# Kernel tuning notes

Hardware: AMD Instinct MI355X
Metric: run time of the kernel (lower is better)

Reference implementation:

```python
import jax, jax.numpy as jnp
import numpy as np

B, T, C, H = 4, 1024, 1024, 16
D = C // H


def setup_inputs() -> dict:
    key = jax.random.key(0)
    ks = jax.random.split(key, 6)
    s = 1.0 / np.sqrt(C)
    return {
        "x": jax.random.normal(ks[0], (B, T, C), jnp.float32),
        "W_qkv": jax.random.normal(ks[1], (C, 3 * C), jnp.float32) * s,
        "b_qkv": jnp.zeros((3 * C,), jnp.float32),
        "W_out": jax.random.normal(ks[2], (C, C), jnp.float32) * s,
        "b_out": jnp.zeros((C,), jnp.float32),
        "w_sur": jax.random.normal(ks[3], (C,), jnp.float32) * s,
        "b_sur": jnp.zeros((), jnp.float32),
        "threshold": jnp.float32(0.5),
    }


def _expmap0_split(u):
    # geoopt Lorentz (k=1) expmap0: first coordinate is the time axis.
    # Minkowski norm of tangent u: sqrt(clamp(-u0^2 + |u_rest|^2, 1e-8))
    mink = -u[..., :1] ** 2 + jnp.sum(u[..., 1:] ** 2, axis=-1, keepdims=True)
    nomin = jnp.sqrt(jnp.maximum(mink, 1e-8))  # [..., 1]
    time = jnp.cosh(nomin)                      # [..., 1]
    space = jnp.sinh(nomin) * u[..., 1:] / nomin  # [..., D-1]
    return time, space


def reference(x, W_qkv, b_qkv, W_out, b_out, w_sur, b_sur, threshold):
    Bx, Tx, Cx = x.shape
    # spiking gate on query rows (causal tril over a (T,1) matrix is all-True -> no-op)
    importance = jax.nn.sigmoid(jnp.einsum("btc,c->bt", x, w_sur) + b_sur)  # [B,T]
    spikes = (importance > threshold).astype(x.dtype)                       # [B,T]
    spike_mask = spikes[:, None, :, None]                                   # [B,1,T,1]

    qkv = x @ W_qkv + b_qkv                                                 # [B,T,3C]
    qkv = qkv.reshape(Bx, Tx, 3, H, D).transpose(2, 0, 3, 1, 4)             # [3,B,H,T,D]
    q, k, v = qkv[0], qkv[1], qkv[2]

    tq, sq = _expmap0_split(q)  # [B,H,T,1], [B,H,T,D-1]
    tk, sk = _expmap0_split(k)
    # -<x,y>_L = tq*tk - <sq,sk>  (pairwise, via matmuls instead of broadcast tensors)
    neg_inner = jnp.einsum("bhie,bhje->bhij", tq, tk) - jnp.einsum(
        "bhid,bhjd->bhij", sq, sk
    )  # [B,H,T,T]
    dist = jnp.arccosh(jnp.maximum(neg_inner, 1.0 + 1e-7))
    scores = -(dist ** 2) / np.sqrt(D)

    causal = jnp.tril(jnp.ones((Tx, Tx), dtype=bool))
    scores = jnp.where(causal[None, None], scores, -jnp.inf)
    attn = jax.nn.softmax(scores, axis=-1) * spike_mask                     # [B,H,T,T]

    y = jnp.einsum("bhij,bhjd->bhid", attn, v)                              # [B,H,T,D]
    y = y.transpose(0, 2, 1, 3).reshape(Bx, Tx, Cx)
    return y @ W_out + b_out
```

## Files before the change

kernel.cpp:

```cpp
#include <hip/hip_runtime.h>
#include <math.h>

#define BB 4
#define TT 1024
#define CC 1024
#define HH 16
#define DD 64
#define NQKV (3 * CC)
#define MROWS (BB * TT)

typedef __attribute__((ext_vector_type(8))) short bf16x8;
typedef __attribute__((ext_vector_type(4))) float f32x4;

struct alignas(8) US4 { unsigned short x, y, z, w; };

__device__ __forceinline__ float b2f(unsigned short u) {
  unsigned int w = ((unsigned int)u) << 16;
  float f; __builtin_memcpy(&f, &w, 4); return f;
}
__device__ __forceinline__ unsigned short f2b(float f) {
  unsigned int u; __builtin_memcpy(&u, &f, 4);
  u += 0x7FFFu + ((u >> 16) & 1);
  return (unsigned short)(u >> 16);
}

__device__ __forceinline__ float hw_log2(float x) {
  return __builtin_amdgcn_logf(x);
}
__device__ __forceinline__ float hw_exp2(float x) {
  return __builtin_amdgcn_exp2f(x);
}

__device__ __forceinline__ void gload16(const void* g, void* l) {
  __builtin_amdgcn_global_load_lds(
      (const __attribute__((address_space(1))) unsigned int*)g,
      (__attribute__((address_space(3))) unsigned int*)l, 16, 0, 0);
}

__device__ __forceinline__ bf16x8 ld_sw(const unsigned short* row_base,
                                        int lc, int rsw) {
  return *(const bf16x8*)((const char*)row_base + (((lc ^ rsw) & 7) << 4));
}

__global__ __launch_bounds__(256) void prep(
    const float* __restrict__ x, const float* __restrict__ w_sur,
    const float* __restrict__ b_sur, const float* __restrict__ thr,
    const float* __restrict__ W_qkv, const float* __restrict__ W_out,
    float* __restrict__ spikes, unsigned short* __restrict__ xb,
    unsigned short* __restrict__ WqkvT, unsigned short* __restrict__ WoutT) {
  __shared__ float t[32][33];
  const int blk = blockIdx.x;

  if (blk < 4096) {
    const float* W; unsigned short* WT; int K, N, bx, by;
    if (blk < 3072) {
      W = W_qkv; WT = WqkvT; K = CC; N = NQKV;
      bx = blk % 96; by = blk / 96;
    } else {
      W = W_out; WT = WoutT; K = CC; N = CC;
      const int b2 = blk - 3072;
      bx = b2 & 31; by = b2 >> 5;
    }
    const int tx = threadIdx.x & 31, ty = threadIdx.x >> 5;
    const int k0 = by * 32, n0 = bx * 32;
#pragma unroll
    for (int i = 0; i < 32; i += 8)
      t[ty + i][tx] = W[(size_t)(k0 + ty + i) * N + n0 + tx];
    __syncthreads();
#pragma unroll
    for (int i = 0; i < 32; i += 8)
      WT[(size_t)(n0 + ty + i) * K + k0 + tx] = f2b(t[tx][ty + i]);
  } else {
    const int row = (blk - 4096) * 4 + (threadIdx.x >> 6);
    const int lane = threadIdx.x & 63;
    const float* xr = x + (size_t)row * CC;
    unsigned short* xo = xb + (size_t)row * CC;
    double acc = 0.0;
#pragma unroll
    for (int s = 0; s < 4; ++s) {
      const int idx = s * 256 + lane * 4;
      const float4 xv = *(const float4*)(xr + idx);
      const float4 wv = *(const float4*)(w_sur + idx);
      acc += (double)xv.x * (double)wv.x;
      acc += (double)xv.y * (double)wv.y;
      acc += (double)xv.z * (double)wv.z;
      acc += (double)xv.w * (double)wv.w;
      US4 o = {f2b(xv.x), f2b(xv.y), f2b(xv.z), f2b(xv.w)};
      *(US4*)(xo + idx) = o;
    }
#pragma unroll
    for (int off = 32; off > 0; off >>= 1) acc += __shfl_xor(acc, off, 64);
    if (lane == 0) {
      const float z = (float)acc + b_sur[0];
      const float imp = 1.0f / (1.0f + __expf(-z));
      spikes[row] = (imp > thr[0]) ? 1.0f : 0.0f;
    }
  }
}

__global__ __launch_bounds__(256, 3) void gemm_qkv(
    const unsigned short* __restrict__ A, const unsigned short* __restrict__ BT,
    const float* __restrict__ bias, unsigned short* __restrict__ qkvb,
    unsigned short* __restrict__ vT) {
  const int K = CC;
  __shared__ unsigned short SH[16384];
  unsigned short (*As)[64] = (unsigned short(*)[64])SH;
  unsigned short (*Bs)[64] = (unsigned short(*)[64])(SH + 8192);
  const int tid = threadIdx.x;
  const int lane = tid & 63;
  const int wave = tid >> 6;
  const int wr = wave >> 1;
  const int wc = wave & 1;
  const int m0 = blockIdx.y * 128;
  const int n0 = blockIdx.x * 128;
  const int ln15 = lane & 15;
  const int g = lane >> 4;
  const int rsw = ln15 & 7;

  const int srow = tid >> 3;
  const int schk = ((tid & 7) ^ (srow & 7)) * 8;
  const unsigned short* gA = A + (size_t)(m0 + srow) * K + schk;
  const unsigned short* gB = BT + (size_t)(n0 + srow) * K + schk;
  char* lA = (char*)SH + wave * 1024;
  char* lB = (char*)SH + 16384 + wave * 1024;

  f32x4 acc[4][4] = {};

  for (int k0 = 0; k0 < K; k0 += 64) {
    __syncthreads();
#pragma unroll
    for (int i = 0; i < 4; ++i)
      gload16(gA + k0 + (size_t)(32 * i) * K, lA + i * 4096);
#pragma unroll
    for (int i = 0; i < 4; ++i)
      gload16(gB + k0 + (size_t)(32 * i) * K, lB + i * 4096);
    __syncthreads();

#pragma unroll
    for (int c = 0; c < 2; ++c) {
      bf16x8 af[4], bfr[4];
#pragma unroll
      for (int i = 0; i < 4; ++i)
        af[i] = ld_sw(&As[wr * 64 + i * 16 + ln15][0], c * 4 + g, rsw);
#pragma unroll
      for (int j = 0; j < 4; ++j)
        bfr[j] = ld_sw(&Bs[wc * 64 + j * 16 + ln15][0], c * 4 + g, rsw);
#pragma unroll
      for (int i = 0; i < 4; ++i)
#pragma unroll
        for (int j = 0; j < 4; ++j)
          acc[i][j] = __builtin_amdgcn_mfma_f32_16x16x32_bf16(
              af[i], bfr[j], acc[i][j], 0, 0, 0);
    }
  }

  __syncthreads();
  unsigned short* scr = SH + wave * 4096;

  const int bx = blockIdx.x;
  if (bx < 16) {
    const bool isk = (bx >= 8);
#pragma unroll
    for (int i = 0; i < 4; ++i) {
#pragma unroll
      for (int r = 0; r < 4; ++r) {
        float u[4];
        float part = 0.f;
#pragma unroll
        for (int j = 0; j < 4; ++j) {
          u[j] = acc[i][j][r] + bias[n0 + wc * 64 + j * 16 + ln15];
          float sq = u[j] * u[j];
          if (j == 0 && ln15 == 0) sq = -sq;
          part += sq;
        }
#pragma unroll
        for (int off = 1; off < 16; off <<= 1)
          part += __shfl_xor(part, off, 64);
        const float nomin = sqrtf(fmaxf(part, 1e-8f));
        const float e = __expf(nomin);
        const float ei = __builtin_amdgcn_rcpf(e);
        const float tim = 0.5f * (e + ei);
        const float coef = 0.5f * (e - ei) * __builtin_amdgcn_rcpf(nomin);
        const int lrow = i * 16 + g * 4 + r;
#pragma unroll
        for (int j = 0; j < 4; ++j) {
          float o = (j == 0 && ln15 == 0) ? tim : coef * u[j];
          if (isk && !(j == 0 && ln15 == 0)) o = -o;
          const int col = j * 16 + ln15;
          const int ch = ((col >> 3) + lrow) & 7;
          scr[lrow * 64 + ch * 8 + (col & 7)] = f2b(o);
        }
      }
    }
#pragma unroll
    for (int it = 0; it < 8; ++it) {
      const int row = (lane >> 3) + 8 * it;
      const int ch = lane & 7;
      const int ph = (ch + row) & 7;
      const bf16x8 v = *(const bf16x8*)&scr[row * 64 + ph * 8];
      *(bf16x8*)&qkvb[(size_t)(m0 + wr * 64 + row) * NQKV + n0 + wc * 64 + ch * 8] = v;
    }
  } else {
#pragma unroll
    for (int i = 0; i < 4; ++i) {
#pragma unroll
      for (int j = 0; j < 4; ++j) {
        const float bb_ = bias[n0 + wc * 64 + j * 16 + ln15];
        const int drow = j * 16 + ln15;
#pragma unroll
        for (int r = 0; r < 4; ++r) {
          const int col = i * 16 + g * 4 + r;
          const int ch = ((col >> 3) + drow) & 7;
          scr[drow * 64 + ch * 8 + (col & 7)] = f2b(acc[i][j][r] + bb_);
        }
      }
    }
    const int hh = (bx - 16) * 2 + wc;
    const int mbase = m0 + wr * 64;
    const int bq = mbase >> 10;
    const int t0 = mbase & 1023;
#pragma unroll
    for (int it = 0; it < 8; ++it) {
      const int drow = (lane >> 3) + 8 * it;
      const int ch = lane & 7;
      const int ph = (ch + drow) & 7;
      const bf16x8 v = *(const bf16x8*)&scr[drow * 64 + ph * 8];
      *(bf16x8*)&vT[((size_t)(bq * HH + hh) * DD + drow) * TT + t0 + ch * 8] = v;
    }
  }
}

__global__ __launch_bounds__(256) void gemm_out(
    const unsigned short* __restrict__ A, const unsigned short* __restrict__ BT,
    const float* __restrict__ bias, float* __restrict__ C) {
  const int N = CC, K = CC;
  __shared__ unsigned short As[128][64];
  __shared__ unsigned short Bs[64][64];
  const int tid = threadIdx.x;
  const int lane = tid & 63;
  const int wave = tid >> 6;
  const int wm = wave * 32;
  const int m0 = blockIdx.y * 128;
  const int n0 = blockIdx.x * 64;
  const int ln15 = lane & 15;
  const int g = lane >> 4;
  const int rsw = ln15 & 7;

  const int srow = tid >> 3;
  const int schk = ((tid & 7) ^ (srow & 7)) * 8;
  const unsigned short* gA = A + (size_t)(m0 + srow) * K + schk;
  const unsigned short* gB = BT + (size_t)(n0 + srow) * K + schk;
  char* lA = (char*)As + wave * 1024;
  char* lB = (char*)Bs + wave * 1024;

  f32x4 acc[2][4] = {};

  for (int k0 = 0; k0 < K; k0 += 64) {
    __syncthreads();
#pragma unroll
    for (int i = 0; i < 4; ++i)
      gload16(gA + k0 + (size_t)(32 * i) * K, lA + i * 4096);
#pragma unroll
    for (int i = 0; i < 2; ++i)
      gload16(gB + k0 + (size_t)(32 * i) * K, lB + i * 4096);
    __syncthreads();

#pragma unroll
    for (int c = 0; c < 2; ++c) {
      bf16x8 af[2], bfr[4];
#pragma unroll
      for (int i = 0; i < 2; ++i)
        af[i] = ld_sw(&As[wm + i * 16 + ln15][0], c * 4 + g, rsw);
#pragma unroll
      for (int j = 0; j < 4; ++j)
        bfr[j] = ld_sw(&Bs[j * 16 + ln15][0], c * 4 + g, rsw);
#pragma unroll
      for (int i = 0; i < 2; ++i)
#pragma unroll
        for (int j = 0; j < 4; ++j)
          acc[i][j] = __builtin_amdgcn_mfma_f32_16x16x32_bf16(
              af[i], bfr[j], acc[i][j], 0, 0, 0);
    }
  }

#pragma unroll
  for (int i = 0; i < 2; ++i) {
#pragma unroll
    for (int r = 0; r < 4; ++r) {
      const int m = m0 + wm + i * 16 + g * 4 + r;
#pragma unroll
      for (int j = 0; j < 4; ++j) {
        const int n = n0 + j * 16 + ln15;
        C[(size_t)m * N + n] = acc[i][j][r] + bias[n];
      }
    }
  }
}

__global__ __launch_bounds__(512) void flash_mfma(
    const unsigned short* __restrict__ qkv, const unsigned short* __restrict__ vT,
    const float* __restrict__ spikes, unsigned short* __restrict__ y) {
  __shared__ unsigned short Ks[128][68];
  __shared__ unsigned short Vs[64][136];
  __shared__ unsigned short Ps[128][68];

  const int tid = threadIdx.x;
  const int lane = tid & 63;
  const int wave = tid >> 6;
  const int ln15 = lane & 15;
  const int g = lane >> 4;
  const int bh = blockIdx.y;
  const int itile = (bh < 32) ? ((int)gridDim.x - 1 - (int)blockIdx.x)
                              : (int)blockIdx.x;
  const int b = bh >> 4;
  const int h = bh & 15;
  const int i0 = itile * 128;
  const int band = wave * 16;
  const int htiles = itile + 1;
  const unsigned short* base = qkv + (size_t)b * TT * NQKV;
  const unsigned short* vbase = vT + (size_t)bh * DD * TT;
  const int qoff = h * DD;
  const int koff = CC + h * DD;

  const int ksn = tid >> 2;
  const int kqc = (tid & 3) * 2;
  const int vsn = tid >> 3;
  const int vqc = (tid & 7) * 2;

  bf16x8 qf[2];
  {
    const unsigned short* qp = base + (size_t)(i0 + band + ln15) * NQKV + qoff;
    qf[0] = *(const bf16x8*)(qp + g * 8);
    qf[1] = *(const bf16x8*)(qp + 32 + g * 8);
  }

  f32x4 accy[4] = {};
  float lrow[4] = {0.f, 0.f, 0.f, 0.f};

  float4 kr0, kr1, vr0, vr1;
  {
    const unsigned short* kp = base + (size_t)ksn * NQKV + koff + kqc * 8;
    const unsigned short* vp = vbase + (size_t)vsn * TT + vqc * 8;
    kr0 = *(const float4*)(kp + 0);
    kr1 = *(const float4*)(kp + 8);
    vr0 = *(const float4*)(vp + 0);
    vr1 = *(const float4*)(vp + 8);
  }

  for (int ht = 0; ht < htiles; ++ht) {
    const int j0h = ht * 128;
    __syncthreads();
    *(float4*)&Ks[ksn][kqc * 8 + 0] = kr0;
    *(float4*)&Ks[ksn][kqc * 8 + 8] = kr1;
    *(float4*)&Vs[vsn][vqc * 8 + 0] = vr0;
    *(float4*)&Vs[vsn][vqc * 8 + 8] = vr1;
    __syncthreads();

    if (ht + 1 < htiles) {
      const int j1 = j0h + 128;
      const unsigned short* kp = base + (size_t)(j1 + ksn) * NQKV + koff + kqc * 8;
      const unsigned short* vp = vbase + (size_t)vsn * TT + j1 + vqc * 8;
      kr0 = *(const float4*)(kp + 0);
      kr1 = *(const float4*)(kp + 8);
      vr0 = *(const float4*)(vp + 0);
      vr1 = *(const float4*)(vp + 8);
    }

#pragma unroll
    for (int t2 = 0; t2 < 2; ++t2) {
      const int j0 = j0h + t2 * 64;
      if (j0 > i0 + band + 15) continue;

      f32x4 sf[4];
      __builtin_amdgcn_s_setprio(1);
#pragma unroll
      for (int j = 0; j < 4; ++j) {
        const bf16x8 k0 = *(const bf16x8*)&Ks[t2 * 64 + j * 16 + ln15][g * 8];
        const bf16x8 k1 = *(const bf16x8*)&Ks[t2 * 64 + j * 16 + ln15][32 + g * 8];
        f32x4 z = {};
        z = __builtin_amdgcn_mfma_f32_16x16x32_bf16(qf[0], k0, z, 0, 0, 0);
        sf[j] = __builtin_amdgcn_mfma_f32_16x16x32_bf16(qf[1], k1, z, 0, 0, 0);
      }
      __builtin_amdgcn_s_setprio(0);

      float p[4][4];
      if (j0 + 63 <= i0 + band) {
#pragma unroll
        for (int j = 0; j < 4; ++j)
#pragma unroll
          for (int r = 0; r < 4; ++r) {
            const float l = hw_log2(fmaxf(sf[j][r], 1.0f));
            const float s = l + 1.0f;
            p[r][j] = hw_exp2(-0.08664339757f * s * s);
          }
      } else {
#pragma unroll
        for (int j = 0; j < 4; ++j) {
          const int gj = j0 + j * 16 + ln15;
#pragma unroll
          for (int r = 0; r < 4; ++r) {
            const int gi = i0 + band + g * 4 + r;
            float e;
            if (gj > gi) {
              e = 0.f;
            } else {
              const float l = hw_log2(fmaxf(sf[j][r], 1.0f));
              const float s = l + 1.0f;
              e = hw_exp2(-0.08664339757f * s * s);
            }
            p[r][j] = e;
          }
        }
      }
#pragma unroll
      for (int r = 0; r < 4; ++r)
        lrow[r] += (p[r][0] + p[r][1]) + (p[r][2] + p[r][3]);

#pragma unroll
      for (int r = 0; r < 4; ++r)
#pragma unroll
        for (int j = 0; j < 4; ++j)
          Ps[band + g * 4 + r][j * 16 + ln15] = f2b(p[r][j]);

      const bf16x8 pa0 = *(const bf16x8*)&Ps[band + ln15][g * 8];
      const bf16x8 pa1 = *(const bf16x8*)&Ps[band + ln15][32 + g * 8];
      __builtin_amdgcn_s_setprio(1);
#pragma unroll
      for (int dt = 0; dt < 4; ++dt) {
        const bf16x8 v0 = *(const bf16x8*)&Vs[dt * 16 + ln15][t2 * 64 + g * 8];
        const bf16x8 v1 = *(const bf16x8*)&Vs[dt * 16 + ln15][t2 * 64 + 32 + g * 8];
        accy[dt] = __builtin_amdgcn_mfma_f32_16x16x32_bf16(pa0, v0, accy[dt], 0, 0, 0);
        accy[dt] = __builtin_amdgcn_mfma_f32_16x16x32_bf16(pa1, v1, accy[dt], 0, 0, 0);
      }
      __builtin_amdgcn_s_setprio(0);
    }
  }

#pragma unroll
  for (int r = 0; r < 4; ++r) {
#pragma unroll
    for (int off = 1; off < 16; off <<= 1)
      lrow[r] += __shfl_xor(lrow[r], off, 64);
  }
  const int grow = b * TT + i0 + band + g * 4;
#pragma unroll
  for (int r = 0; r < 4; ++r) {
    const float spk = spikes[grow + r];
    const float scale = spk / lrow[r];
#pragma unroll
    for (int dt = 0; dt < 4; ++dt)
      y[(size_t)(grow + r) * CC + h * DD + dt * 16 + ln15] =
          f2b(accy[dt][r] * scale);
  }
}

extern "C" void kernel_launch(void* const* d_in, const int* in_sizes, int n_in,
                              void* d_out, int out_size, void* d_ws, size_t ws_size,
                              hipStream_t stream) {
  const float* x     = (const float*)d_in[0];
  const float* W_qkv = (const float*)d_in[1];
  const float* b_qkv = (const float*)d_in[2];
  const float* W_out = (const float*)d_in[3];
  const float* b_out = (const float*)d_in[4];
  const float* w_sur = (const float*)d_in[5];
  const float* b_sur = (const float*)d_in[6];
  const float* thr   = (const float*)d_in[7];
  float* out = (float*)d_out;

  char* w = (char*)d_ws;
  unsigned short* xb    = (unsigned short*)(w);
  unsigned short* qkvb  = (unsigned short*)(w + 8388608);
  unsigned short* vTb   = (unsigned short*)(w + 8388608 + 25165824);
  unsigned short* ybufb = (unsigned short*)(w + 8388608 + 25165824 + 8388608);
  unsigned short* WqkvT = (unsigned short*)(w + 8388608 + 25165824 + 2 * 8388608);
  unsigned short* WoutT = (unsigned short*)(w + 8388608 + 25165824 + 2 * 8388608 + 6291456);
  float* spikes = (float*)(w + 8388608 + 25165824 + 2 * 8388608 + 6291456 + 2097152);

  prep<<<5120, 256, 0, stream>>>(x, w_sur, b_sur, thr, W_qkv, W_out,
                                 spikes, xb, WqkvT, WoutT);

  gemm_qkv<<<dim3(NQKV / 128, MROWS / 128), 256, 0, stream>>>(
      xb, WqkvT, b_qkv, qkvb, vTb);

  flash_mfma<<<dim3(TT / 128, BB * HH), 512, 0, stream>>>(qkvb, vTb, spikes, ybufb);

  gemm_out<<<dim3(CC / 64, MROWS / 128), 256, 0, stream>>>(
      ybufb, WoutT, b_out, out);
}
```

Before: 164.8 us.

## Compact spiking rows and skip Q-projection and output GEMM for silent rows

```diff
diff --git a/kernel.cpp b/kernel.cpp
--- a/kernel.cpp
+++ b/kernel.cpp
@@ -14,6 +14,8 @@
 
 struct alignas(8) US4 { unsigned short x, y, z, w; };
 
+__device__ __forceinline__ int imin(int a, int b) { return a < b ? a : b; }
+
 __device__ __forceinline__ float b2f(unsigned short u) {
   unsigned int w = ((unsigned int)u) << 16;
   float f; __builtin_memcpy(&f, &w, 4); return f;
@@ -46,6 +48,7 @@
     const float* __restrict__ x, const float* __restrict__ w_sur,
     const float* __restrict__ b_sur, const float* __restrict__ thr,
     const float* __restrict__ W_qkv, const float* __restrict__ W_out,
+    const float* __restrict__ b_out, float* __restrict__ out,
     float* __restrict__ spikes, unsigned short* __restrict__ xb,
     unsigned short* __restrict__ WqkvT, unsigned short* __restrict__ WoutT) {
   __shared__ float t[32][33];
@@ -90,17 +93,60 @@
     }
 #pragma unroll
     for (int off = 32; off > 0; off >>= 1) acc += __shfl_xor(acc, off, 64);
+    float spk = 0.f;
     if (lane == 0) {
       const float z = (float)acc + b_sur[0];
       const float imp = 1.0f / (1.0f + __expf(-z));
-      spikes[row] = (imp > thr[0]) ? 1.0f : 0.0f;
-    }
-  }
+      spk = (imp > thr[0]) ? 1.0f : 0.0f;
+      spikes[row] = spk;
+    }
+    spk = __shfl(spk, 0, 64);
+    if (spk == 0.f) {
+      float* orow = out + (size_t)row * CC;
+#pragma unroll
+      for (int s = 0; s < 4; ++s) {
+        const int idx = s * 256 + lane * 4;
+        *(float4*)(orow + idx) = *(const float4*)(b_out + idx);
+      }
+    }
+  }
+}
+
+__global__ __launch_bounds__(1024) void compact(
+    const float* __restrict__ spikes, unsigned short* __restrict__ cidx,
+    int* __restrict__ cntp) {
+  const int tid = threadIdx.x;
+  const int lane = tid & 63, wv = tid >> 6;
+  __shared__ int wsum[16];
+  __shared__ int woff[16];
+  __shared__ int sbase;
+  if (tid == 0) sbase = 0;
+  __syncthreads();
+#pragma unroll
+  for (int p = 0; p < 4; ++p) {
+    const int row = p * 1024 + tid;
+    const bool f = spikes[row] > 0.5f;
+    const unsigned long long bal = __ballot(f);
+    const int wpre = __popcll(bal & ((1ull << lane) - 1ull));
+    if (lane == 0) wsum[wv] = __popcll(bal);
+    __syncthreads();
+    if (tid == 0) {
+      int s = sbase;
+#pragma unroll
+      for (int i = 0; i < 16; ++i) { woff[i] = s; s += wsum[i]; }
+      sbase = s;
+    }
+    __syncthreads();
+    if (f) cidx[woff[wv] + wpre] = (unsigned short)row;
+    __syncthreads();
+  }
+  if (tid == 0) cntp[0] = sbase;
 }
 
 __global__ __launch_bounds__(256, 3) void gemm_qkv(
     const unsigned short* __restrict__ A, const unsigned short* __restrict__ BT,
-    const float* __restrict__ bias, unsigned short* __restrict__ qkvb,
+    const float* __restrict__ bias, const unsigned short* __restrict__ cidx,
+    const int* __restrict__ cntp, unsigned short* __restrict__ qkvb,
     unsigned short* __restrict__ vT) {
   const int K = CC;
   __shared__ unsigned short SH[16384];
@@ -113,13 +159,24 @@
   const int wc = wave & 1;
   const int m0 = blockIdx.y * 128;
   const int n0 = blockIdx.x * 128;
+  const int bx = blockIdx.x;
   const int ln15 = lane & 15;
   const int g = lane >> 4;
   const int rsw = ln15 & 7;
 
+  const bool isq = (bx < 8);
+  const int cnt = cntp[0];
+  if (isq && m0 >= cnt) return;
+
   const int srow = tid >> 3;
   const int schk = ((tid & 7) ^ (srow & 7)) * 8;
-  const unsigned short* gA = A + (size_t)(m0 + srow) * K + schk;
+  const unsigned short* gAr[4];
+#pragma unroll
+  for (int i = 0; i < 4; ++i) {
+    int row = m0 + srow + 32 * i;
+    if (isq) row = (int)cidx[imin(row, cnt - 1)];
+    gAr[i] = A + (size_t)row * K + schk;
+  }
   const unsigned short* gB = BT + (size_t)(n0 + srow) * K + schk;
   char* lA = (char*)SH + wave * 1024;
   char* lB = (char*)SH + 16384 + wave * 1024;
@@ -130,7 +187,7 @@
     __syncthreads();
 #pragma unroll
     for (int i = 0; i < 4; ++i)
-      gload16(gA + k0 + (size_t)(32 * i) * K, lA + i * 4096);
+      gload16(gAr[i] + k0, lA + i * 4096);
 #pragma unroll
     for (int i = 0; i < 4; ++i)
       gload16(gB + k0 + (size_t)(32 * i) * K, lB + i * 4096);
@@ -157,7 +214,6 @@
   __syncthreads();
   unsigned short* scr = SH + wave * 4096;
 
-  const int bx = blockIdx.x;
   if (bx < 16) {
     const bool isk = (bx >= 8);
 #pragma unroll
@@ -198,7 +254,12 @@
       const int ch = lane & 7;
       const int ph = (ch + row) & 7;
       const bf16x8 v = *(const bf16x8*)&scr[row * 64 + ph * 8];
-      *(bf16x8*)&qkvb[(size_t)(m0 + wr * 64 + row) * NQKV + n0 + wc * 64 + ch * 8] = v;
+      int orow = m0 + wr * 64 + row;
+      if (isq) {
+        if (orow >= cnt) continue;
+        orow = (int)cidx[orow];
+      }
+      *(bf16x8*)&qkvb[(size_t)orow * NQKV + n0 + wc * 64 + ch * 8] = v;
     }
   } else {
 #pragma unroll
@@ -232,7 +293,8 @@
 
 __global__ __launch_bounds__(256) void gemm_out(
     const unsigned short* __restrict__ A, const unsigned short* __restrict__ BT,
-    const float* __restrict__ bias, float* __restrict__ C) {
+    const float* __restrict__ bias, const unsigned short* __restrict__ cidx,
+    const int* __restrict__ cntp, float* __restrict__ C) {
   const int N = CC, K = CC;
   __shared__ unsigned short As[128][64];
   __shared__ unsigned short Bs[64][64];
@@ -246,9 +308,17 @@
   const int g = lane >> 4;
   const int rsw = ln15 & 7;
 
+  const int cnt = cntp[0];
+  if (m0 >= cnt) return;
+
   const int srow = tid >> 3;
   const int schk = ((tid & 7) ^ (srow & 7)) * 8;
-  const unsigned short* gA = A + (size_t)(m0 + srow) * K + schk;
+  const unsigned short* gAr[4];
+#pragma unroll
+  for (int i = 0; i < 4; ++i) {
+    const int row = (int)cidx[imin(m0 + srow + 32 * i, cnt - 1)];
+    gAr[i] = A + (size_t)row * K + schk;
+  }
   const unsigned short* gB = BT + (size_t)(n0 + srow) * K + schk;
   char* lA = (char*)As + wave * 1024;
   char* lB = (char*)Bs + wave * 1024;
@@ -259,7 +329,7 @@
     __syncthreads();
 #pragma unroll
     for (int i = 0; i < 4; ++i)
-      gload16(gA + k0 + (size_t)(32 * i) * K, lA + i * 4096);
+      gload16(gAr[i] + k0, lA + i * 4096);
 #pragma unroll
     for (int i = 0; i < 2; ++i)
       gload16(gB + k0 + (size_t)(32 * i) * K, lB + i * 4096);
@@ -287,11 +357,14 @@
   for (int i = 0; i < 2; ++i) {
 #pragma unroll
     for (int r = 0; r < 4; ++r) {
-      const int m = m0 + wm + i * 16 + g * 4 + r;
-#pragma unroll
-      for (int j = 0; j < 4; ++j) {
-        const int n = n0 + j * 16 + ln15;
-        C[(size_t)m * N + n] = acc[i][j][r] + bias[n];
+      const int mslot = m0 + wm + i * 16 + g * 4 + r;
+      if (mslot < cnt) {
+        const int m = (int)cidx[mslot];
+#pragma unroll
+        for (int j = 0; j < 4; ++j) {
+          const int n = n0 + j * 16 + ln15;
+          C[(size_t)m * N + n] = acc[i][j][r] + bias[n];
+        }
       }
     }
   }
@@ -474,16 +547,20 @@
   unsigned short* ybufb = (unsigned short*)(w + 8388608 + 25165824 + 8388608);
   unsigned short* WqkvT = (unsigned short*)(w + 8388608 + 25165824 + 2 * 8388608);
   unsigned short* WoutT = (unsigned short*)(w + 8388608 + 25165824 + 2 * 8388608 + 6291456);
-  float* spikes = (float*)(w + 8388608 + 25165824 + 2 * 8388608 + 6291456 + 2097152);
+  float* spikes = (float*)(w + 58720256);
+  unsigned short* cidx = (unsigned short*)(w + 58720256 + 16384);
+  int* cnt = (int*)(w + 58720256 + 16384 + 8192);
 
   prep<<<5120, 256, 0, stream>>>(x, w_sur, b_sur, thr, W_qkv, W_out,
-                                 spikes, xb, WqkvT, WoutT);
+                                 b_out, out, spikes, xb, WqkvT, WoutT);
+
+  compact<<<1, 1024, 0, stream>>>(spikes, cidx, cnt);
 
   gemm_qkv<<<dim3(NQKV / 128, MROWS / 128), 256, 0, stream>>>(
-      xb, WqkvT, b_qkv, qkvb, vTb);
+      xb, WqkvT, b_qkv, cidx, cnt, qkvb, vTb);
 
   flash_mfma<<<dim3(TT / 128, BB * HH), 512, 0, stream>>>(qkvb, vTb, spikes, ybufb);
 
   gemm_out<<<dim3(CC / 64, MROWS / 128), 256, 0, stream>>>(
-      ybufb, WoutT, b_out, out);
-}
+      ybufb, WoutT, b_out, cidx, cnt, out);
+}
```

After: 170.9 us. 1.04x slower.
